# Optimization experiments

Measured on AMD Instinct MI355X. Metric: run time of the kernel, lower is better.

Reference implementation:

```python
import jax, jax.numpy as jnp
import numpy as np

LEVEL = 3  # J
B3_TAPS = (1.0 / 16, 1.0 / 4, 3.0 / 8, 1.0 / 4, 1.0 / 16)  # h1, fixed non-trainable


def _b3_conv2d(x, d):
    """Separable 5-tap B3-spline conv with dilation d and reflect padding.

    Equivalent to torch Conv2d(1,1,5,dilation=d,padding=2*d,padding_mode='reflect')
    with weight = outer(h1, h1): the dense 5x5 kernel is separable.
    x: (B, H, W) -> (B, H, W)
    """
    w = [jnp.asarray(t, x.dtype) for t in B3_TAPS]
    pad = 2 * d  # effective half-width of dilated 5-tap kernel
    H, W = x.shape[1], x.shape[2]
    # conv along H
    xp = jnp.pad(x, ((0, 0), (pad, pad), (0, 0)), mode='reflect')
    x = sum(w[k] * xp[:, k * d:k * d + H, :] for k in range(5))
    # conv along W
    xp = jnp.pad(x, ((0, 0), (0, 0), (pad, pad)), mode='reflect')
    x = sum(w[k] * xp[:, :, k * d:k * d + W] for k in range(5))
    return x


def setup_inputs() -> dict:
    key = jax.random.key(0)
    x = jax.random.normal(key, (8, 1024, 1024), dtype=jnp.float32)
    return {"x": x}


def reference(x) -> jnp.ndarray:
    # c_j = h_j * c_{j-1};  w_j = c_{j-1} - c_j;  return [w_1..w_J, c_J] stacked on axis 1
    outs = []
    c = x
    for j in range(LEVEL):
        c_next = _b3_conv2d(c, 2 ** j)
        outs.append(c - c_next)
        c = c_next
    outs.append(c)
    return jnp.stack(outs, axis=1)  # (B, J+1, H, W)
```

## Files before the change

kernel.cpp:

```cpp
#include <hip/hip_runtime.h>

#define DEVINL __device__ __forceinline__


constexpr int W_IMG = 1024;
constexpr int H_IMG = 1024;
constexpr int TX = 32;
constexpr int TY = 64;
constexpr int HALO = 16;
constexpr int SW = 68;
constexpr int SH = TY + 2 * HALO;
constexpr int GXT = W_IMG / TX;
constexpr int GYT = H_IMG / TY;

constexpr float TP0 = 1.0f / 16.0f;
constexpr float TP1 = 1.0f / 4.0f;
constexpr float TP2 = 3.0f / 8.0f;

typedef float f32x4 __attribute__((ext_vector_type(4)));

template <int CTRL>
DEVINL float dppf(float x) {
    return __int_as_float(__builtin_amdgcn_update_dpp(
        0, __float_as_int(x), CTRL, 0xF, 0xF, true));
}

DEVINL int reflx(int g) {
    g = g < 0 ? -g : g;
    return g >= W_IMG ? 2 * W_IMG - 2 - g : g;
}

DEVINL void nt_store4(float* p, float a, float b, float c, float d) {
    f32x4 t;
    t.x = a; t.y = b; t.z = c; t.w = d;
    __builtin_nontemporal_store(t, (f32x4*)p);
}

template <int D, int R0, int R1, int LVL, bool LAST>
DEVINL void do_level(const float* src, float* dst, float* __restrict__ out,
                     int b4, int oy0, int gx0, int p, int ty) {
    const int c4 = p * 4;
    constexpr int KMAX = (R1 - R0 + 15) / 16;
#pragma unroll 2
    for (int k = 0; k < KMAX; ++k) {
        const int r = R0 + ty + 16 * k;
        if (r < R1) {
            const float4 a0 = *(const float4*)&src[(r - 2 * D) * SW + c4];
            const float4 a1 = *(const float4*)&src[(r - D) * SW + c4];
            const float4 a2 = *(const float4*)&src[r * SW + c4];
            const float4 a3 = *(const float4*)&src[(r + D) * SW + c4];
            const float4 a4 = *(const float4*)&src[(r + 2 * D) * SW + c4];
            float4 v;
            v.x = TP0 * (a0.x + a4.x) + TP1 * (a1.x + a3.x) + TP2 * a2.x;
            v.y = TP0 * (a0.y + a4.y) + TP1 * (a1.y + a3.y) + TP2 * a2.y;
            v.z = TP0 * (a0.z + a4.z) + TP1 * (a1.z + a3.z) + TP2 * a2.z;
            v.w = TP0 * (a0.w + a4.w) + TP1 * (a1.w + a3.w) + TP2 * a2.w;
            float4 u;
            if constexpr (D == 1) {
                const float am2 = dppf<0x111>(v.z);
                const float am1 = dppf<0x111>(v.w);
                const float ap1 = dppf<0x101>(v.x);
                const float ap2 = dppf<0x101>(v.y);
                u.x = TP0 * (am2 + v.z) + TP1 * (am1 + v.y) + TP2 * v.x;
                u.y = TP0 * (am1 + v.w) + TP1 * (v.x + v.z) + TP2 * v.y;
                u.z = TP0 * (v.x + ap1) + TP1 * (v.y + v.w) + TP2 * v.z;
                u.w = TP0 * (v.y + ap2) + TP1 * (v.z + ap1) + TP2 * v.w;
            } else if constexpr (D == 2) {
                u.x = TP0 * (dppf<0x111>(v.x) + dppf<0x101>(v.x)) +
                      TP1 * (dppf<0x111>(v.z) + v.z) + TP2 * v.x;
                u.y = TP0 * (dppf<0x111>(v.y) + dppf<0x101>(v.y)) +
                      TP1 * (dppf<0x111>(v.w) + v.w) + TP2 * v.y;
                u.z = TP0 * (dppf<0x111>(v.z) + dppf<0x101>(v.z)) +
                      TP1 * (v.x + dppf<0x101>(v.x)) + TP2 * v.z;
                u.w = TP0 * (dppf<0x111>(v.w) + dppf<0x101>(v.w)) +
                      TP1 * (v.y + dppf<0x101>(v.y)) + TP2 * v.w;
            } else {
                u.x = TP0 * (dppf<0x112>(v.x) + dppf<0x102>(v.x)) +
                      TP1 * (dppf<0x111>(v.x) + dppf<0x101>(v.x)) + TP2 * v.x;
                u.y = TP0 * (dppf<0x112>(v.y) + dppf<0x102>(v.y)) +
                      TP1 * (dppf<0x111>(v.y) + dppf<0x101>(v.y)) + TP2 * v.y;
                u.z = TP0 * (dppf<0x112>(v.z) + dppf<0x102>(v.z)) +
                      TP1 * (dppf<0x111>(v.z) + dppf<0x101>(v.z)) + TP2 * v.z;
                u.w = TP0 * (dppf<0x112>(v.w) + dppf<0x102>(v.w)) +
                      TP1 * (dppf<0x111>(v.w) + dppf<0x101>(v.w)) + TP2 * v.w;
            }
            const int ly = r - HALO;
            const int oy = oy0 + ly;
            if ((unsigned)ly < (unsigned)TY && p >= 4 && p < 12) {
                const int ox = gx0 + c4 - HALO;
                const size_t base =
                    ((size_t)(b4 + LVL) * H_IMG + oy) * W_IMG + ox;
                nt_store4(&out[base], a2.x - u.x, a2.y - u.y, a2.z - u.z,
                          a2.w - u.w);
                if constexpr (LAST) {
                    const size_t base3 =
                        ((size_t)(b4 + 3) * H_IMG + oy) * W_IMG + ox;
                    nt_store4(&out[base3], u.x, u.y, u.z, u.w);
                }
            }
            if constexpr (!LAST) *(float4*)&dst[r * SW + c4] = u;
        }
    }
}

__global__ __launch_bounds__(256, 3) void uwt3(const float* __restrict__ x,
                                               float* __restrict__ out) {
    __shared__ __align__(16) float A[SH * SW];
    __shared__ __align__(16) float B[SH * SW];

    const int tid = threadIdx.x;
    const int p = tid & 15;
    const int ty = tid >> 4;
    int bid = blockIdx.x;
    const int bx = bid & 31;  bid >>= 5;
    const int by = bid & 15;
    const int b = bid >> 4;
    const int oy0 = by * TY;
    const int gx0 = bx * TX;
    const float* xb = x + (size_t)b * (H_IMG * W_IMG);
    const int c4 = p * 4;
    const bool edge = (bx == 0) || (bx == GXT - 1);

#pragma unroll 2
    for (int k = 0; k < SH / 16; ++k) {
        const int sr = ty + 16 * k;
        int gy = oy0 - HALO + sr;
        gy = gy < 0 ? -gy : gy;
        if (gy >= H_IMG) gy = 2 * H_IMG - 2 - gy;
        const float* row = xb + (size_t)gy * W_IMG;
        const int gx = gx0 - HALO + c4;
        float4 v;
        if (!edge) {
            v = *(const float4*)(row + gx);
        } else {
            v.x = row[reflx(gx)];
            v.y = row[reflx(gx + 1)];
            v.z = row[reflx(gx + 2)];
            v.w = row[reflx(gx + 3)];
        }
        *(float4*)&A[sr * SW + c4] = v;
    }
    __syncthreads();

    do_level<1, 4, 92, 0, false>(A, B, out, b * 4, oy0, gx0, p, ty);
    __syncthreads();
    do_level<2, 8, 88, 1, false>(B, A, out, b * 4, oy0, gx0, p, ty);
    __syncthreads();
    do_level<4, 16, 80, 2, true>(A, B, out, b * 4, oy0, gx0, p, ty);
}

extern "C" void kernel_launch(void* const* d_in, const int* in_sizes, int n_in,
                              void* d_out, int out_size, void* d_ws,
                              size_t ws_size, hipStream_t stream) {
    const float* x = (const float*)d_in[0];
    float* out = (float*)d_out;
    const int nb = in_sizes[0] / (H_IMG * W_IMG);
    dim3 grid(nb * GYT * GXT);
    uwt3<<<grid, 256, 0, stream>>>(x, out);
}
```

Baseline: 179.3 us.

## Assign contiguous row bands per thread with sliding-window register reuse of LDS rows

```diff
diff --git a/kernel.cpp b/kernel.cpp
--- a/kernel.cpp
+++ b/kernel.cpp
@@ -36,69 +36,143 @@
     __builtin_nontemporal_store(t, (f32x4*)p);
 }
 
-template <int D, int R0, int R1, int LVL, bool LAST>
-DEVINL void do_level(const float* src, float* dst, float* __restrict__ out,
-                     int b4, int oy0, int gx0, int p, int ty) {
-    const int c4 = p * 4;
-    constexpr int KMAX = (R1 - R0 + 15) / 16;
-#pragma unroll 2
-    for (int k = 0; k < KMAX; ++k) {
-        const int r = R0 + ty + 16 * k;
-        if (r < R1) {
-            const float4 a0 = *(const float4*)&src[(r - 2 * D) * SW + c4];
-            const float4 a1 = *(const float4*)&src[(r - D) * SW + c4];
-            const float4 a2 = *(const float4*)&src[r * SW + c4];
-            const float4 a3 = *(const float4*)&src[(r + D) * SW + c4];
-            const float4 a4 = *(const float4*)&src[(r + 2 * D) * SW + c4];
-            float4 v;
-            v.x = TP0 * (a0.x + a4.x) + TP1 * (a1.x + a3.x) + TP2 * a2.x;
-            v.y = TP0 * (a0.y + a4.y) + TP1 * (a1.y + a3.y) + TP2 * a2.y;
-            v.z = TP0 * (a0.z + a4.z) + TP1 * (a1.z + a3.z) + TP2 * a2.z;
-            v.w = TP0 * (a0.w + a4.w) + TP1 * (a1.w + a3.w) + TP2 * a2.w;
-            float4 u;
-            if constexpr (D == 1) {
-                const float am2 = dppf<0x111>(v.z);
-                const float am1 = dppf<0x111>(v.w);
-                const float ap1 = dppf<0x101>(v.x);
-                const float ap2 = dppf<0x101>(v.y);
-                u.x = TP0 * (am2 + v.z) + TP1 * (am1 + v.y) + TP2 * v.x;
-                u.y = TP0 * (am1 + v.w) + TP1 * (v.x + v.z) + TP2 * v.y;
-                u.z = TP0 * (v.x + ap1) + TP1 * (v.y + v.w) + TP2 * v.z;
-                u.w = TP0 * (v.y + ap2) + TP1 * (v.z + ap1) + TP2 * v.w;
-            } else if constexpr (D == 2) {
-                u.x = TP0 * (dppf<0x111>(v.x) + dppf<0x101>(v.x)) +
-                      TP1 * (dppf<0x111>(v.z) + v.z) + TP2 * v.x;
-                u.y = TP0 * (dppf<0x111>(v.y) + dppf<0x101>(v.y)) +
-                      TP1 * (dppf<0x111>(v.w) + v.w) + TP2 * v.y;
-                u.z = TP0 * (dppf<0x111>(v.z) + dppf<0x101>(v.z)) +
-                      TP1 * (v.x + dppf<0x101>(v.x)) + TP2 * v.z;
-                u.w = TP0 * (dppf<0x111>(v.w) + dppf<0x101>(v.w)) +
-                      TP1 * (v.y + dppf<0x101>(v.y)) + TP2 * v.w;
-            } else {
-                u.x = TP0 * (dppf<0x112>(v.x) + dppf<0x102>(v.x)) +
-                      TP1 * (dppf<0x111>(v.x) + dppf<0x101>(v.x)) + TP2 * v.x;
-                u.y = TP0 * (dppf<0x112>(v.y) + dppf<0x102>(v.y)) +
-                      TP1 * (dppf<0x111>(v.y) + dppf<0x101>(v.y)) + TP2 * v.y;
-                u.z = TP0 * (dppf<0x112>(v.z) + dppf<0x102>(v.z)) +
-                      TP1 * (dppf<0x111>(v.z) + dppf<0x101>(v.z)) + TP2 * v.z;
-                u.w = TP0 * (dppf<0x112>(v.w) + dppf<0x102>(v.w)) +
-                      TP1 * (dppf<0x111>(v.w) + dppf<0x101>(v.w)) + TP2 * v.w;
-            }
-            const int ly = r - HALO;
-            const int oy = oy0 + ly;
-            if ((unsigned)ly < (unsigned)TY && p >= 4 && p < 12) {
-                const int ox = gx0 + c4 - HALO;
-                const size_t base =
-                    ((size_t)(b4 + LVL) * H_IMG + oy) * W_IMG + ox;
-                nt_store4(&out[base], a2.x - u.x, a2.y - u.y, a2.z - u.z,
-                          a2.w - u.w);
-                if constexpr (LAST) {
-                    const size_t base3 =
-                        ((size_t)(b4 + 3) * H_IMG + oy) * W_IMG + ox;
-                    nt_store4(&out[base3], u.x, u.y, u.z, u.w);
-                }
-            }
-            if constexpr (!LAST) *(float4*)&dst[r * SW + c4] = u;
+DEVINL float4 vert(const float4& a0, const float4& a1, const float4& a2,
+                   const float4& a3, const float4& a4) {
+    float4 v;
+    v.x = TP0 * (a0.x + a4.x) + TP1 * (a1.x + a3.x) + TP2 * a2.x;
+    v.y = TP0 * (a0.y + a4.y) + TP1 * (a1.y + a3.y) + TP2 * a2.y;
+    v.z = TP0 * (a0.z + a4.z) + TP1 * (a1.z + a3.z) + TP2 * a2.z;
+    v.w = TP0 * (a0.w + a4.w) + TP1 * (a1.w + a3.w) + TP2 * a2.w;
+    return v;
+}
+
+template <int D>
+DEVINL float4 horiz(const float4& v) {
+    float4 u;
+    if constexpr (D == 1) {
+        const float am2 = dppf<0x111>(v.z);
+        const float am1 = dppf<0x111>(v.w);
+        const float ap1 = dppf<0x101>(v.x);
+        const float ap2 = dppf<0x101>(v.y);
+        u.x = TP0 * (am2 + v.z) + TP1 * (am1 + v.y) + TP2 * v.x;
+        u.y = TP0 * (am1 + v.w) + TP1 * (v.x + v.z) + TP2 * v.y;
+        u.z = TP0 * (v.x + ap1) + TP1 * (v.y + v.w) + TP2 * v.z;
+        u.w = TP0 * (v.y + ap2) + TP1 * (v.z + ap1) + TP2 * v.w;
+    } else if constexpr (D == 2) {
+        u.x = TP0 * (dppf<0x111>(v.x) + dppf<0x101>(v.x)) +
+              TP1 * (dppf<0x111>(v.z) + v.z) + TP2 * v.x;
+        u.y = TP0 * (dppf<0x111>(v.y) + dppf<0x101>(v.y)) +
+              TP1 * (dppf<0x111>(v.w) + v.w) + TP2 * v.y;
+        u.z = TP0 * (dppf<0x111>(v.z) + dppf<0x101>(v.z)) +
+              TP1 * (v.x + dppf<0x101>(v.x)) + TP2 * v.z;
+        u.w = TP0 * (dppf<0x111>(v.w) + dppf<0x101>(v.w)) +
+              TP1 * (v.y + dppf<0x101>(v.y)) + TP2 * v.w;
+    } else {
+        u.x = TP0 * (dppf<0x112>(v.x) + dppf<0x102>(v.x)) +
+              TP1 * (dppf<0x111>(v.x) + dppf<0x101>(v.x)) + TP2 * v.x;
+        u.y = TP0 * (dppf<0x112>(v.y) + dppf<0x102>(v.y)) +
+              TP1 * (dppf<0x111>(v.y) + dppf<0x101>(v.y)) + TP2 * v.y;
+        u.z = TP0 * (dppf<0x112>(v.z) + dppf<0x102>(v.z)) +
+              TP1 * (dppf<0x111>(v.z) + dppf<0x101>(v.z)) + TP2 * v.z;
+        u.w = TP0 * (dppf<0x112>(v.w) + dppf<0x102>(v.w)) +
+              TP1 * (dppf<0x111>(v.w) + dppf<0x101>(v.w)) + TP2 * v.w;
+    }
+    return u;
+}
+
+template <int LVL, bool ALSO_C>
+DEVINL void maybe_store(float* __restrict__ out, int b4, int oy0, int gx0,
+                        int p, int r, const float4& center, const float4& u) {
+    const int ly = r - HALO;
+    if ((unsigned)ly < (unsigned)TY && p >= 4 && p < 12) {
+        const int oy = oy0 + ly;
+        const int ox = gx0 + p * 4 - HALO;
+        const size_t base = ((size_t)(b4 + LVL) * H_IMG + oy) * W_IMG + ox;
+        nt_store4(&out[base], center.x - u.x, center.y - u.y, center.z - u.z,
+                  center.w - u.w);
+        if constexpr (ALSO_C) {
+            const size_t base3 = ((size_t)(b4 + 3) * H_IMG + oy) * W_IMG + ox;
+            nt_store4(&out[base3], u.x, u.y, u.z, u.w);
+        }
+    }
+}
+
+DEVINL void level0(const float* src, float* dst, float* __restrict__ out,
+                   int b4, int oy0, int gx0, int p, int ty) {
+    const int c4 = p * 4;
+    const int r0 = ty < 8 ? 4 + 6 * ty : 52 + 5 * (ty - 8);
+    const int band = ty < 8 ? 6 : 5;
+    const float* base = &src[r0 * SW + c4];
+    float4 w0 = *(const float4*)(base - 2 * SW);
+    float4 w1 = *(const float4*)(base - 1 * SW);
+    float4 w2 = *(const float4*)(base);
+    float4 w3 = *(const float4*)(base + 1 * SW);
+#pragma unroll
+    for (int k = 0; k < 6; ++k) {
+        if (k < band) {
+            const float4 w4 = *(const float4*)(base + (k + 2) * SW);
+            const float4 v = vert(w0, w1, w2, w3, w4);
+            const float4 u = horiz<1>(v);
+            maybe_store<0, false>(out, b4, oy0, gx0, p, r0 + k, w2, u);
+            *(float4*)&dst[(r0 + k) * SW + c4] = u;
+            w0 = w1; w1 = w2; w2 = w3; w3 = w4;
+        }
+    }
+}
+
+DEVINL void step_d2(const float* base, int off, float4& q0, float4& q1,
+                    float4& q2, float4& q3, float* dst,
+                    float* __restrict__ out, int b4, int oy0, int gx0, int p,
+                    int r) {
+    const float4 q4 = *(const float4*)(base + off * SW);
+    const float4 v = vert(q0, q1, q2, q3, q4);
+    const float4 u = horiz<2>(v);
+    maybe_store<1, false>(out, b4, oy0, gx0, p, r, q2, u);
+    *(float4*)&dst[r * SW + p * 4] = u;
+    q0 = q1; q1 = q2; q2 = q3; q3 = q4;
+}
+
+DEVINL void level1(const float* src, float* dst, float* __restrict__ out,
+                   int b4, int oy0, int gx0, int p, int ty) {
+    const int c4 = p * 4;
+    const int r0 = 8 + 5 * ty;
+    const float* base = &src[r0 * SW + c4];
+    float4 a0 = *(const float4*)(base - 4 * SW);
+    float4 a1 = *(const float4*)(base - 2 * SW);
+    float4 a2 = *(const float4*)(base);
+    float4 a3 = *(const float4*)(base + 2 * SW);
+    float4 b0 = *(const float4*)(base - 3 * SW);
+    float4 b1 = *(const float4*)(base - 1 * SW);
+    float4 b2 = *(const float4*)(base + 1 * SW);
+    float4 b3 = *(const float4*)(base + 3 * SW);
+    step_d2(base, 4, a0, a1, a2, a3, dst, out, b4, oy0, gx0, p, r0);
+    step_d2(base, 5, b0, b1, b2, b3, dst, out, b4, oy0, gx0, p, r0 + 1);
+    step_d2(base, 6, a0, a1, a2, a3, dst, out, b4, oy0, gx0, p, r0 + 2);
+    step_d2(base, 7, b0, b1, b2, b3, dst, out, b4, oy0, gx0, p, r0 + 3);
+    step_d2(base, 8, a0, a1, a2, a3, dst, out, b4, oy0, gx0, p, r0 + 4);
+}
+
+DEVINL void level2(const float* src, float* __restrict__ out, int b4, int oy0,
+                   int gx0, int p, int ty) {
+    const int c4 = p * 4;
+#pragma unroll
+    for (int k = 0; k < 4; ++k) {
+        const int r = 16 + ty + 16 * k;
+        const float4 a0 = *(const float4*)&src[(r - 8) * SW + c4];
+        const float4 a1 = *(const float4*)&src[(r - 4) * SW + c4];
+        const float4 a2 = *(const float4*)&src[r * SW + c4];
+        const float4 a3 = *(const float4*)&src[(r + 4) * SW + c4];
+        const float4 a4 = *(const float4*)&src[(r + 8) * SW + c4];
+        const float4 v = vert(a0, a1, a2, a3, a4);
+        const float4 u = horiz<4>(v);
+        if (p >= 4 && p < 12) {
+            const int oy = oy0 + r - HALO;
+            const int ox = gx0 + c4 - HALO;
+            const size_t base = ((size_t)(b4 + 2) * H_IMG + oy) * W_IMG + ox;
+            nt_store4(&out[base], a2.x - u.x, a2.y - u.y, a2.z - u.z,
+                      a2.w - u.w);
+            const size_t base3 = ((size_t)(b4 + 3) * H_IMG + oy) * W_IMG + ox;
+            nt_store4(&out[base3], u.x, u.y, u.z, u.w);
         }
     }
 }
@@ -121,32 +195,34 @@
     const int c4 = p * 4;
     const bool edge = (bx == 0) || (bx == GXT - 1);
 
-#pragma unroll 2
-    for (int k = 0; k < SH / 16; ++k) {
-        const int sr = ty + 16 * k;
-        int gy = oy0 - HALO + sr;
-        gy = gy < 0 ? -gy : gy;
-        if (gy >= H_IMG) gy = 2 * H_IMG - 2 - gy;
-        const float* row = xb + (size_t)gy * W_IMG;
-        const int gx = gx0 - HALO + c4;
-        float4 v;
-        if (!edge) {
-            v = *(const float4*)(row + gx);
-        } else {
-            v.x = row[reflx(gx)];
-            v.y = row[reflx(gx + 1)];
-            v.z = row[reflx(gx + 2)];
-            v.w = row[reflx(gx + 3)];
-        }
-        *(float4*)&A[sr * SW + c4] = v;
+#pragma unroll
+    for (int k = 0; k < 6; ++k) {
+        const int sr = 2 + ty + 16 * k;
+        if (sr < 94) {
+            int gy = oy0 - HALO + sr;
+            gy = gy < 0 ? -gy : gy;
+            if (gy >= H_IMG) gy = 2 * H_IMG - 2 - gy;
+            const float* row = xb + (size_t)gy * W_IMG;
+            const int gx = gx0 - HALO + c4;
+            float4 v;
+            if (!edge) {
+                v = *(const float4*)(row + gx);
+            } else {
+                v.x = row[reflx(gx)];
+                v.y = row[reflx(gx + 1)];
+                v.z = row[reflx(gx + 2)];
+                v.w = row[reflx(gx + 3)];
+            }
+            *(float4*)&A[sr * SW + c4] = v;
+        }
     }
     __syncthreads();
 
-    do_level<1, 4, 92, 0, false>(A, B, out, b * 4, oy0, gx0, p, ty);
+    level0(A, B, out, b * 4, oy0, gx0, p, ty);
     __syncthreads();
-    do_level<2, 8, 88, 1, false>(B, A, out, b * 4, oy0, gx0, p, ty);
+    level1(B, A, out, b * 4, oy0, gx0, p, ty);
     __syncthreads();
-    do_level<4, 16, 80, 2, true>(A, B, out, b * 4, oy0, gx0, p, ty);
+    level2(A, out, b * 4, oy0, gx0, p, ty);
 }
 
 extern "C" void kernel_launch(void* const* d_in, const int* in_sizes, int n_in,
```

Result: no change. 182.3 us (+1.6%).

## Compute multiple output rows per thread to reuse LDS loads across vertical taps

Applied to the files above, without the earlier changes.

```diff
diff --git a/kernel.cpp b/kernel.cpp
--- a/kernel.cpp
+++ b/kernel.cpp
@@ -9,7 +9,7 @@
 constexpr int TY = 64;
 constexpr int HALO = 16;
 constexpr int SW = 68;
-constexpr int SH = TY + 2 * HALO;
+constexpr int SH = 96;
 constexpr int GXT = W_IMG / TX;
 constexpr int GYT = H_IMG / TY;
 
@@ -36,71 +36,133 @@
     __builtin_nontemporal_store(t, (f32x4*)p);
 }
 
-template <int D, int R0, int R1, int LVL, bool LAST>
-DEVINL void do_level(const float* src, float* dst, float* __restrict__ out,
-                     int b4, int oy0, int gx0, int p, int ty) {
-    const int c4 = p * 4;
-    constexpr int KMAX = (R1 - R0 + 15) / 16;
+DEVINL float4 ld4(const float* p) { return *(const float4*)p; }
+
+DEVINL float4 vert(const float4& a0, const float4& a1, const float4& a2,
+                   const float4& a3, const float4& a4) {
+    float4 v;
+    v.x = TP0 * (a0.x + a4.x) + TP1 * (a1.x + a3.x) + TP2 * a2.x;
+    v.y = TP0 * (a0.y + a4.y) + TP1 * (a1.y + a3.y) + TP2 * a2.y;
+    v.z = TP0 * (a0.z + a4.z) + TP1 * (a1.z + a3.z) + TP2 * a2.z;
+    v.w = TP0 * (a0.w + a4.w) + TP1 * (a1.w + a3.w) + TP2 * a2.w;
+    return v;
+}
+
+template <int D>
+DEVINL float4 horiz(const float4& v) {
+    float4 u;
+    if constexpr (D == 1) {
+        const float am2 = dppf<0x111>(v.z);
+        const float am1 = dppf<0x111>(v.w);
+        const float ap1 = dppf<0x101>(v.x);
+        const float ap2 = dppf<0x101>(v.y);
+        u.x = TP0 * (am2 + v.z) + TP1 * (am1 + v.y) + TP2 * v.x;
+        u.y = TP0 * (am1 + v.w) + TP1 * (v.x + v.z) + TP2 * v.y;
+        u.z = TP0 * (v.x + ap1) + TP1 * (v.y + v.w) + TP2 * v.z;
+        u.w = TP0 * (v.y + ap2) + TP1 * (v.z + ap1) + TP2 * v.w;
+    } else if constexpr (D == 2) {
+        u.x = TP0 * (dppf<0x111>(v.x) + dppf<0x101>(v.x)) +
+              TP1 * (dppf<0x111>(v.z) + v.z) + TP2 * v.x;
+        u.y = TP0 * (dppf<0x111>(v.y) + dppf<0x101>(v.y)) +
+              TP1 * (dppf<0x111>(v.w) + v.w) + TP2 * v.y;
+        u.z = TP0 * (dppf<0x111>(v.z) + dppf<0x101>(v.z)) +
+              TP1 * (v.x + dppf<0x101>(v.x)) + TP2 * v.z;
+        u.w = TP0 * (dppf<0x111>(v.w) + dppf<0x101>(v.w)) +
+              TP1 * (v.y + dppf<0x101>(v.y)) + TP2 * v.w;
+    } else {
+        u.x = TP0 * (dppf<0x112>(v.x) + dppf<0x102>(v.x)) +
+              TP1 * (dppf<0x111>(v.x) + dppf<0x101>(v.x)) + TP2 * v.x;
+        u.y = TP0 * (dppf<0x112>(v.y) + dppf<0x102>(v.y)) +
+              TP1 * (dppf<0x111>(v.y) + dppf<0x101>(v.y)) + TP2 * v.y;
+        u.z = TP0 * (dppf<0x112>(v.z) + dppf<0x102>(v.z)) +
+              TP1 * (dppf<0x111>(v.z) + dppf<0x101>(v.z)) + TP2 * v.z;
+        u.w = TP0 * (dppf<0x112>(v.w) + dppf<0x102>(v.w)) +
+              TP1 * (dppf<0x111>(v.w) + dppf<0x101>(v.w)) + TP2 * v.w;
+    }
+    return u;
+}
+
+template <int LVL, bool ALSO_C>
+DEVINL void st(float* obase, bool pok, int ly, const float4& c,
+               const float4& u) {
+    if (pok && (unsigned)ly < (unsigned)TY) {
+        constexpr size_t PL = (size_t)H_IMG * W_IMG;
+        float* pw = obase + (size_t)LVL * PL + (size_t)ly * W_IMG;
+        nt_store4(pw, c.x - u.x, c.y - u.y, c.z - u.z, c.w - u.w);
+        if constexpr (ALSO_C) {
+            float* pc = obase + (size_t)3 * PL + (size_t)ly * W_IMG;
+            nt_store4(pc, u.x, u.y, u.z, u.w);
+        }
+    }
+}
+
+DEVINL void level0(const float* src, float* dst, float* obase, bool pok,
+                   int ty, int c4) {
 #pragma unroll 2
-    for (int k = 0; k < KMAX; ++k) {
-        const int r = R0 + ty + 16 * k;
-        if (r < R1) {
-            const float4 a0 = *(const float4*)&src[(r - 2 * D) * SW + c4];
-            const float4 a1 = *(const float4*)&src[(r - D) * SW + c4];
-            const float4 a2 = *(const float4*)&src[r * SW + c4];
-            const float4 a3 = *(const float4*)&src[(r + D) * SW + c4];
-            const float4 a4 = *(const float4*)&src[(r + 2 * D) * SW + c4];
-            float4 v;
-            v.x = TP0 * (a0.x + a4.x) + TP1 * (a1.x + a3.x) + TP2 * a2.x;
-            v.y = TP0 * (a0.y + a4.y) + TP1 * (a1.y + a3.y) + TP2 * a2.y;
-            v.z = TP0 * (a0.z + a4.z) + TP1 * (a1.z + a3.z) + TP2 * a2.z;
-            v.w = TP0 * (a0.w + a4.w) + TP1 * (a1.w + a3.w) + TP2 * a2.w;
-            float4 u;
-            if constexpr (D == 1) {
-                const float am2 = dppf<0x111>(v.z);
-                const float am1 = dppf<0x111>(v.w);
-                const float ap1 = dppf<0x101>(v.x);
-                const float ap2 = dppf<0x101>(v.y);
-                u.x = TP0 * (am2 + v.z) + TP1 * (am1 + v.y) + TP2 * v.x;
-                u.y = TP0 * (am1 + v.w) + TP1 * (v.x + v.z) + TP2 * v.y;
-                u.z = TP0 * (v.x + ap1) + TP1 * (v.y + v.w) + TP2 * v.z;
-                u.w = TP0 * (v.y + ap2) + TP1 * (v.z + ap1) + TP2 * v.w;
-            } else if constexpr (D == 2) {
-                u.x = TP0 * (dppf<0x111>(v.x) + dppf<0x101>(v.x)) +
-                      TP1 * (dppf<0x111>(v.z) + v.z) + TP2 * v.x;
-                u.y = TP0 * (dppf<0x111>(v.y) + dppf<0x101>(v.y)) +
-                      TP1 * (dppf<0x111>(v.w) + v.w) + TP2 * v.y;
-                u.z = TP0 * (dppf<0x111>(v.z) + dppf<0x101>(v.z)) +
-                      TP1 * (v.x + dppf<0x101>(v.x)) + TP2 * v.z;
-                u.w = TP0 * (dppf<0x111>(v.w) + dppf<0x101>(v.w)) +
-                      TP1 * (v.y + dppf<0x101>(v.y)) + TP2 * v.w;
-            } else {
-                u.x = TP0 * (dppf<0x112>(v.x) + dppf<0x102>(v.x)) +
-                      TP1 * (dppf<0x111>(v.x) + dppf<0x101>(v.x)) + TP2 * v.x;
-                u.y = TP0 * (dppf<0x112>(v.y) + dppf<0x102>(v.y)) +
-                      TP1 * (dppf<0x111>(v.y) + dppf<0x101>(v.y)) + TP2 * v.y;
-                u.z = TP0 * (dppf<0x112>(v.z) + dppf<0x102>(v.z)) +
-                      TP1 * (dppf<0x111>(v.z) + dppf<0x101>(v.z)) + TP2 * v.z;
-                u.w = TP0 * (dppf<0x112>(v.w) + dppf<0x102>(v.w)) +
-                      TP1 * (dppf<0x111>(v.w) + dppf<0x101>(v.w)) + TP2 * v.w;
-            }
-            const int ly = r - HALO;
-            const int oy = oy0 + ly;
-            if ((unsigned)ly < (unsigned)TY && p >= 4 && p < 12) {
-                const int ox = gx0 + c4 - HALO;
-                const size_t base =
-                    ((size_t)(b4 + LVL) * H_IMG + oy) * W_IMG + ox;
-                nt_store4(&out[base], a2.x - u.x, a2.y - u.y, a2.z - u.z,
-                          a2.w - u.w);
-                if constexpr (LAST) {
-                    const size_t base3 =
-                        ((size_t)(b4 + 3) * H_IMG + oy) * W_IMG + ox;
-                    nt_store4(&out[base3], u.x, u.y, u.z, u.w);
-                }
-            }
-            if constexpr (!LAST) *(float4*)&dst[r * SW + c4] = u;
-        }
-    }
+    for (int k = 0; k < 3; ++k) {
+        const int pi = ty + 16 * k;
+        if (pi < 44) {
+            const int r = 4 + 2 * pi;
+            const float* b = &src[r * SW + c4];
+            const float4 m2 = ld4(b - 2 * SW);
+            const float4 m1 = ld4(b - 1 * SW);
+            const float4 z0 = ld4(b);
+            const float4 z1 = ld4(b + 1 * SW);
+            const float4 z2 = ld4(b + 2 * SW);
+            const float4 z3 = ld4(b + 3 * SW);
+            const float4 u0 = horiz<1>(vert(m2, m1, z0, z1, z2));
+            const float4 u1 = horiz<1>(vert(m1, z0, z1, z2, z3));
+            st<0, false>(obase, pok, r - HALO, z0, u0);
+            st<0, false>(obase, pok, r + 1 - HALO, z1, u1);
+            *(float4*)&dst[r * SW + c4] = u0;
+            *(float4*)&dst[(r + 1) * SW + c4] = u1;
+        }
+    }
+}
+
+DEVINL void level1(const float* src, float* dst, float* obase, bool pok,
+                   int ty, int c4) {
+#pragma unroll 2
+    for (int k = 0; k < 3; ++k) {
+        const int pi = ty + 16 * k;
+        if (pi < 40) {
+            const int r = 8 + (pi & 1) + 4 * (pi >> 1);
+            const float* b = &src[r * SW + c4];
+            const float4 m4 = ld4(b - 4 * SW);
+            const float4 m2 = ld4(b - 2 * SW);
+            const float4 z0 = ld4(b);
+            const float4 z2 = ld4(b + 2 * SW);
+            const float4 z4 = ld4(b + 4 * SW);
+            const float4 z6 = ld4(b + 6 * SW);
+            const float4 u0 = horiz<2>(vert(m4, m2, z0, z2, z4));
+            const float4 u1 = horiz<2>(vert(m2, z0, z2, z4, z6));
+            st<1, false>(obase, pok, r - HALO, z0, u0);
+            st<1, false>(obase, pok, r + 2 - HALO, z2, u1);
+            *(float4*)&dst[r * SW + c4] = u0;
+            *(float4*)&dst[(r + 2) * SW + c4] = u1;
+        }
+    }
+}
+
+DEVINL void level2(const float* src, float* obase, bool pok, int ty, int c4) {
+    const int r0 = 16 + (ty & 3) + 16 * (ty >> 2);
+    const float* b = &src[r0 * SW + c4];
+    const float4 q0 = ld4(b - 8 * SW);
+    const float4 q1 = ld4(b - 4 * SW);
+    const float4 q2 = ld4(b);
+    const float4 q3 = ld4(b + 4 * SW);
+    const float4 q4 = ld4(b + 8 * SW);
+    const float4 q5 = ld4(b + 12 * SW);
+    const float4 q6 = ld4(b + 16 * SW);
+    const float4 q7 = ld4(b + 20 * SW);
+    const float4 u0 = horiz<4>(vert(q0, q1, q2, q3, q4));
+    const float4 u1 = horiz<4>(vert(q1, q2, q3, q4, q5));
+    const float4 u2 = horiz<4>(vert(q2, q3, q4, q5, q6));
+    const float4 u3 = horiz<4>(vert(q3, q4, q5, q6, q7));
+    st<2, true>(obase, pok, r0 - HALO, q2, u0);
+    st<2, true>(obase, pok, r0 + 4 - HALO, q3, u1);
+    st<2, true>(obase, pok, r0 + 8 - HALO, q4, u2);
+    st<2, true>(obase, pok, r0 + 12 - HALO, q5, u3);
 }
 
 __global__ __launch_bounds__(256, 3) void uwt3(const float* __restrict__ x,
@@ -120,33 +182,38 @@
     const float* xb = x + (size_t)b * (H_IMG * W_IMG);
     const int c4 = p * 4;
     const bool edge = (bx == 0) || (bx == GXT - 1);
+    const bool pok = (p >= 4) && (p < 12);
+    float* obase = out + ((size_t)(b * 4) * H_IMG + oy0) * W_IMG +
+                   (gx0 + c4 - HALO);
 
 #pragma unroll 2
-    for (int k = 0; k < SH / 16; ++k) {
-        const int sr = ty + 16 * k;
-        int gy = oy0 - HALO + sr;
-        gy = gy < 0 ? -gy : gy;
-        if (gy >= H_IMG) gy = 2 * H_IMG - 2 - gy;
-        const float* row = xb + (size_t)gy * W_IMG;
-        const int gx = gx0 - HALO + c4;
-        float4 v;
-        if (!edge) {
-            v = *(const float4*)(row + gx);
-        } else {
-            v.x = row[reflx(gx)];
-            v.y = row[reflx(gx + 1)];
-            v.z = row[reflx(gx + 2)];
-            v.w = row[reflx(gx + 3)];
-        }
-        *(float4*)&A[sr * SW + c4] = v;
+    for (int k = 0; k < 6; ++k) {
+        const int sr = 2 + ty + 16 * k;
+        if (sr < 94) {
+            int gy = oy0 - HALO + sr;
+            gy = gy < 0 ? -gy : gy;
+            if (gy >= H_IMG) gy = 2 * H_IMG - 2 - gy;
+            const float* row = xb + (size_t)gy * W_IMG;
+            const int gx = gx0 - HALO + c4;
+            float4 v;
+            if (!edge) {
+                v = *(const float4*)(row + gx);
+            } else {
+                v.x = row[reflx(gx)];
+                v.y = row[reflx(gx + 1)];
+                v.z = row[reflx(gx + 2)];
+                v.w = row[reflx(gx + 3)];
+            }
+            *(float4*)&A[sr * SW + c4] = v;
+        }
     }
     __syncthreads();
 
-    do_level<1, 4, 92, 0, false>(A, B, out, b * 4, oy0, gx0, p, ty);
+    level0(A, B, obase, pok, ty, c4);
     __syncthreads();
-    do_level<2, 8, 88, 1, false>(B, A, out, b * 4, oy0, gx0, p, ty);
+    level1(B, A, obase, pok, ty, c4);
     __syncthreads();
-    do_level<4, 16, 80, 2, true>(A, B, out, b * 4, oy0, gx0, p, ty);
+    level2(A, obase, pok, ty, c4);
 }
 
 extern "C" void kernel_launch(void* const* d_in, const int* in_sizes, int n_in,
```

New measurement: 183.1 us. 2.1% more time.
